# Kernel optimization log

Measured on AMD Instinct MI355X. Metric: run time of the kernel, lower is better.

Reference implementation:

```python
import jax, jax.numpy as jnp
import numpy as np

N_NODES = 50000
N_EDGES = 600000
N_GRAPHS = 512
HID = 128
N_CLASSES = 10
N_LAYERS = 4
BN_EPS = 1e-5


def setup_inputs() -> dict:
    key = jax.random.key(0)
    ks = jax.random.split(key, 12)
    s = 1.0 / np.sqrt(HID)
    x = jax.random.normal(ks[0], (N_NODES, HID), dtype=jnp.float32)
    edge_index = jax.random.randint(ks[1], (2, N_EDGES), 0, N_NODES, dtype=jnp.int64)
    batch = jnp.sort(jax.random.randint(ks[2], (N_NODES,), 0, N_GRAPHS, dtype=jnp.int64))
    return {
        "x": x,
        "edge_index": edge_index,
        "batch": batch,
        # stacked SAGEConv params: lin_l (neighbor, with bias) and lin_r (root, no bias)
        "Wl": jax.random.uniform(ks[3], (N_LAYERS, HID, HID), jnp.float32, -s, s),
        "bl": jax.random.uniform(ks[4], (N_LAYERS, HID), jnp.float32, -s, s),
        "Wr": jax.random.uniform(ks[5], (N_LAYERS, HID, HID), jnp.float32, -s, s),
        # BatchNorm affine params per layer
        "gamma": jnp.ones((N_LAYERS, HID), jnp.float32),
        "beta": jnp.zeros((N_LAYERS, HID), jnp.float32),
        # classifier: Linear(HID, HID//2) -> ReLU -> Linear(HID//2, C)
        "W1": jax.random.uniform(ks[6], (HID // 2, HID), jnp.float32, -s, s),
        "b1": jax.random.uniform(ks[7], (HID // 2,), jnp.float32, -s, s),
        "W2": jax.random.uniform(ks[8], (N_CLASSES, HID // 2), jnp.float32, -1.0 / np.sqrt(HID // 2), 1.0 / np.sqrt(HID // 2)),
        "b2": jax.random.uniform(ks[9], (N_CLASSES,), jnp.float32, -1.0 / np.sqrt(HID // 2), 1.0 / np.sqrt(HID // 2)),
    }


def reference(x, edge_index, batch, Wl, bl, Wr, gamma, beta, W1, b1, W2, b2):
    src, dst = edge_index[0], edge_index[1]
    n = x.shape[0]
    # in-degree for mean aggregation (clamped to avoid div by zero)
    deg = jax.ops.segment_sum(jnp.ones(src.shape[0], x.dtype), dst, num_segments=n)
    inv_deg = 1.0 / jnp.maximum(deg, 1.0)  # [N]
    for l in range(Wl.shape[0]):
        # SAGEConv: mean-aggregate neighbor features, then lin_l(agg) + lin_r(x)
        agg = jax.ops.segment_sum(x[src], dst, num_segments=n) * inv_deg[:, None]  # [N,H]
        h = agg @ Wl[l].T + bl[l] + x @ Wr[l].T  # [N,H]
        # BatchNorm1d (training-mode batch stats, biased variance)
        mu = h.mean(axis=0)
        var = h.var(axis=0)
        h = (h - mu) * jax.lax.rsqrt(var + BN_EPS) * gamma[l] + beta[l]
        x = jax.nn.relu(h)  # dropout is identity in eval/reference
    # global mean pool over graphs
    cnt = jax.ops.segment_sum(jnp.ones(n, x.dtype), batch, num_segments=N_GRAPHS)
    pooled = jax.ops.segment_sum(x, batch, num_segments=N_GRAPHS) / jnp.maximum(cnt, 1.0)[:, None]
    h = jax.nn.relu(pooled @ W1.T + b1)
    return h @ W2.T + b2  # [G, C]
```

## Files before the change

### kernel.cpp

```cpp
#include <hip/hip_runtime.h>

#define NNODES 50000
#define MPAD   50048
#define NEDGES 600000
#define NGRAPHS 512
#define HID 128
#define NLAYERS 4
#define BN_EPS 1e-5f
#define GEMMBLK 391
#define PROWS 25

typedef __bf16 bf16x8 __attribute__((ext_vector_type(8)));
typedef float  f32x4  __attribute__((ext_vector_type(4)));
typedef unsigned short u16x8 __attribute__((ext_vector_type(8)));

__device__ __forceinline__ unsigned short f2bf(float f) {
    unsigned u = __builtin_bit_cast(unsigned, f);
    unsigned r = (u + 0x7fffu + ((u >> 16) & 1u)) >> 16;
    return (unsigned short)r;
}
__device__ __forceinline__ float bf2f(unsigned short u) {
    return __builtin_bit_cast(float, (unsigned)u << 16);
}

__global__ void k_count_deg(const int* __restrict__ dst, int* __restrict__ deg, int E) {
    int e = blockIdx.x * blockDim.x + threadIdx.x;
    if (e < E) atomicAdd(&deg[dst[e]], 1);
}

__global__ void k_scan1(const int* __restrict__ deg, int* __restrict__ exg,
                        int* __restrict__ bsum, int n) {
    __shared__ int s[512];
    int tid = threadIdx.x;
    int i = blockIdx.x * 512 + tid;
    int v = (i < n) ? deg[i] : 0;
    s[tid] = v;
    __syncthreads();
    for (int off = 1; off < 512; off <<= 1) {
        int t = (tid >= off) ? s[tid - off] : 0;
        __syncthreads();
        s[tid] += t;
        __syncthreads();
    }
    if (i < n) exg[i] = s[tid] - v;
    if (tid == 511) bsum[blockIdx.x] = s[511];
}

__global__ void k_scan2(int* __restrict__ bsum, int nb) {
    __shared__ int s[128];
    int tid = threadIdx.x;
    int v = (tid < nb) ? bsum[tid] : 0;
    s[tid] = v;
    __syncthreads();
    for (int off = 1; off < 128; off <<= 1) {
        int t = (tid >= off) ? s[tid - off] : 0;
        __syncthreads();
        s[tid] += t;
        __syncthreads();
    }
    if (tid < nb) bsum[tid] = s[tid] - v;
}

__global__ void k_scan3(const int* __restrict__ exg, const int* __restrict__ bsum,
                        const int* __restrict__ deg,
                        int* __restrict__ rowptr, int* __restrict__ cursor,
                        float* __restrict__ inv_deg, int n, int E) {
    int i = blockIdx.x * blockDim.x + threadIdx.x;
    if (i < n) {
        int r = exg[i] + bsum[i >> 9];
        rowptr[i] = r;
        cursor[i] = r;
        int d = deg[i];
        inv_deg[i] = 1.0f / (float)max(d, 1);
        if (i == 0) rowptr[n] = E;
    }
}

__global__ void k_fill_csr(const int* __restrict__ src, const int* __restrict__ dst,
                           int* __restrict__ cursor, int* __restrict__ csr_src, int E) {
    int e = blockIdx.x * blockDim.x + threadIdx.x;
    if (e < E) {
        int pos = atomicAdd(&cursor[dst[e]], 1);
        csr_src[pos] = src[e];
    }
}

__global__ void k_split(const float* __restrict__ x,
                        unsigned short* __restrict__ xhi, unsigned short* __restrict__ xlo) {
    int idx = blockIdx.x * 256 + threadIdx.x;
    float4 v = ((const float4*)x)[idx];
    ushort4 h, l;
    h.x = f2bf(v.x); l.x = f2bf(v.x - bf2f(h.x));
    h.y = f2bf(v.y); l.y = f2bf(v.y - bf2f(h.y));
    h.z = f2bf(v.z); l.z = f2bf(v.z - bf2f(h.z));
    h.w = f2bf(v.w); l.w = f2bf(v.w - bf2f(h.w));
    *(ushort4*)(xhi + (size_t)idx * 4) = h;
    *(ushort4*)(xlo + (size_t)idx * 4) = l;
}

__global__ void k_wpack(const float* __restrict__ Wl, const float* __restrict__ Wr,
                        unsigned short* __restrict__ Wpk) {
    int lane = threadIdx.x;
    int b = blockIdx.x;
    int nf = b & 7, ks = (b >> 3) & 7, l = b >> 6;
    int n = nf * 16 + (lane & 15);
    int k = ks * 32 + (lane >> 4) * 8;
    const float* W = (k < 128) ? (Wl + (size_t)l * HID * HID)
                               : (Wr + (size_t)l * HID * HID - 128);
    size_t base = ((((size_t)l * 64 + ks * 8 + nf) * 2) * 64 + lane) * 8;
    #pragma unroll
    for (int j = 0; j < 8; ++j) {
        float w = W[(size_t)n * 128 + k + j];
        unsigned short h = f2bf(w);
        unsigned short lo = f2bf(w - bf2f(h));
        Wpk[base + j] = h;
        Wpk[base + 512 + j] = lo;
    }
}

__global__ void k_aggregate4(const unsigned short* __restrict__ xhi,
                             const int* __restrict__ csr_src, const int* __restrict__ rowptr,
                             const float* __restrict__ inv_deg,
                             unsigned short* __restrict__ ahi, unsigned short* __restrict__ alo) {
    int lane = threadIdx.x & 63;
    int wid = threadIdx.x >> 6;
    int node = blockIdx.x * 4 + wid;
    int beg = rowptr[node];
    int end = rowptr[node + 1];
    int eg = lane >> 4;
    int fo = (lane & 15) * 8;
    float acc[8] = {0.f, 0.f, 0.f, 0.f, 0.f, 0.f, 0.f, 0.f};
    int e = beg;
    for (; e + 4 <= end; e += 4) {
        int s = csr_src[e + eg];
        u16x8 v = *(const u16x8*)(xhi + (size_t)s * 128 + fo);
        #pragma unroll
        for (int j = 0; j < 8; ++j) acc[j] += bf2f(v[j]);
    }
    int rem = end - e;
    if (eg < rem) {
        int s = csr_src[e + eg];
        u16x8 v = *(const u16x8*)(xhi + (size_t)s * 128 + fo);
        #pragma unroll
        for (int j = 0; j < 8; ++j) acc[j] += bf2f(v[j]);
    }
    #pragma unroll
    for (int j = 0; j < 8; ++j) {
        acc[j] += __shfl_xor(acc[j], 16);
        acc[j] += __shfl_xor(acc[j], 32);
    }
    if (lane < 16) {
        float idg = inv_deg[node];
        u16x8 hv, lv;
        #pragma unroll
        for (int j = 0; j < 8; ++j) {
            float a = acc[j] * idg;
            unsigned short h = f2bf(a);
            hv[j] = h;
            lv[j] = f2bf(a - bf2f(h));
        }
        *(u16x8*)(ahi + (size_t)node * 128 + fo) = hv;
        *(u16x8*)(alo + (size_t)node * 128 + fo) = lv;
    }
}

__launch_bounds__(256) __global__
void k_mfma_gemm(const unsigned short* __restrict__ Ahi0, const unsigned short* __restrict__ Alo0,
                 const unsigned short* __restrict__ Ahi1, const unsigned short* __restrict__ Alo1,
                 const unsigned short* __restrict__ Wpk, const float* __restrict__ bl,
                 float* __restrict__ Hout,
                 float* __restrict__ psum, float* __restrict__ pqsum) {
    int wid = threadIdx.x >> 6;
    int lane = threadIdx.x & 63;
    int m0 = blockIdx.x * 128 + wid * 32;
    int r = lane & 15;
    int kg = lane >> 4;

    f32x4 acc[2][8];
    #pragma unroll
    for (int nf = 0; nf < 8; ++nf) {
        float b = bl[nf * 16 + r];
        acc[0][nf] = f32x4{b, b, b, b};
        acc[1][nf] = f32x4{b, b, b, b};
    }

    #pragma unroll
    for (int ks = 0; ks < 8; ++ks) {
        const unsigned short* hi = (ks < 4) ? Ahi0 : Ahi1;
        const unsigned short* lo = (ks < 4) ? Alo0 : Alo1;
        int kc = (ks & 3) * 32 + kg * 8;
        bf16x8 ah0 = *(const bf16x8*)(hi + (size_t)(m0 + r) * 128 + kc);
        bf16x8 al0 = *(const bf16x8*)(lo + (size_t)(m0 + r) * 128 + kc);
        bf16x8 ah1 = *(const bf16x8*)(hi + (size_t)(m0 + 16 + r) * 128 + kc);
        bf16x8 al1 = *(const bf16x8*)(lo + (size_t)(m0 + 16 + r) * 128 + kc);
        const unsigned short* wb = Wpk + (size_t)ks * 8192;
        #pragma unroll
        for (int nf = 0; nf < 8; ++nf) {
            bf16x8 bh = *(const bf16x8*)(wb + (size_t)nf * 1024 + lane * 8);
            bf16x8 bl2 = *(const bf16x8*)(wb + (size_t)nf * 1024 + 512 + lane * 8);
            acc[0][nf] = __builtin_amdgcn_mfma_f32_16x16x32_bf16(ah0, bh,  acc[0][nf], 0, 0, 0);
            acc[0][nf] = __builtin_amdgcn_mfma_f32_16x16x32_bf16(al0, bh,  acc[0][nf], 0, 0, 0);
            acc[0][nf] = __builtin_amdgcn_mfma_f32_16x16x32_bf16(ah0, bl2, acc[0][nf], 0, 0, 0);
            acc[1][nf] = __builtin_amdgcn_mfma_f32_16x16x32_bf16(ah1, bh,  acc[1][nf], 0, 0, 0);
            acc[1][nf] = __builtin_amdgcn_mfma_f32_16x16x32_bf16(al1, bh,  acc[1][nf], 0, 0, 0);
            acc[1][nf] = __builtin_amdgcn_mfma_f32_16x16x32_bf16(ah1, bl2, acc[1][nf], 0, 0, 0);
        }
    }

    #pragma unroll
    for (int mf = 0; mf < 2; ++mf)
        #pragma unroll
        for (int nf = 0; nf < 8; ++nf)
            #pragma unroll
            for (int g = 0; g < 4; ++g)
                Hout[(size_t)(m0 + mf * 16 + kg * 4 + g) * 128 + nf * 16 + r] = acc[mf][nf][g];

    __shared__ float ls[4][8][16];
    __shared__ float lq[4][8][16];
    #pragma unroll
    for (int nf = 0; nf < 8; ++nf) {
        float ss = 0.f, qq = 0.f;
        #pragma unroll
        for (int mf = 0; mf < 2; ++mf)
            #pragma unroll
            for (int g = 0; g < 4; ++g) {
                int row = m0 + mf * 16 + kg * 4 + g;
                float v = acc[mf][nf][g];
                float msk = (row < NNODES) ? 1.f : 0.f;
                ss += v * msk;
                qq += v * v * msk;
            }
        ss += __shfl_xor(ss, 16);
        ss += __shfl_xor(ss, 32);
        qq += __shfl_xor(qq, 16);
        qq += __shfl_xor(qq, 32);
        if (lane < 16) { ls[wid][nf][lane] = ss; lq[wid][nf][lane] = qq; }
    }
    __syncthreads();
    int t = threadIdx.x;
    if (t < 128) {
        int nf = t >> 4, rr = t & 15;
        float ssum = ls[0][nf][rr] + ls[1][nf][rr] + ls[2][nf][rr] + ls[3][nf][rr];
        float qsum = lq[0][nf][rr] + lq[1][nf][rr] + lq[2][nf][rr] + lq[3][nf][rr];
        psum[(size_t)t * GEMMBLK + blockIdx.x] = ssum;
        pqsum[(size_t)t * GEMMBLK + blockIdx.x] = qsum;
    }
}

__global__ void k_bnfin2(const float* __restrict__ psum, const float* __restrict__ pqsum,
                         const float* __restrict__ gamma, const float* __restrict__ beta,
                         float* __restrict__ scale, float* __restrict__ shift) {
    int c = blockIdx.x;
    int t = threadIdx.x;
    float s = 0.f, q = 0.f;
    const float* ps = psum + (size_t)c * GEMMBLK;
    const float* pq = pqsum + (size_t)c * GEMMBLK;
    for (int b = t; b < GEMMBLK; b += 64) { s += ps[b]; q += pq[b]; }
    #pragma unroll
    for (int off = 32; off; off >>= 1) {
        s += __shfl_xor(s, off);
        q += __shfl_xor(q, off);
    }
    if (t == 0) {
        float inv_n = 1.0f / (float)NNODES;
        float mu = s * inv_n;
        float var = q * inv_n - mu * mu;
        float is = rsqrtf(var + BN_EPS);
        float g = gamma[c] * is;
        scale[c] = g;
        shift[c] = beta[c] - mu * g;
    }
}

__global__ void k_bnrelu2(const float* __restrict__ h, const float* __restrict__ scale,
                          const float* __restrict__ shift,
                          unsigned short* __restrict__ xhi, unsigned short* __restrict__ xlo) {
    int idx = blockIdx.x * 256 + threadIdx.x;
    int cv = idx & 31;
    float4 sc = ((const float4*)scale)[cv];
    float4 sh = ((const float4*)shift)[cv];
    float4 v = ((const float4*)h)[idx];
    v.x = fmaxf(v.x * sc.x + sh.x, 0.f);
    v.y = fmaxf(v.y * sc.y + sh.y, 0.f);
    v.z = fmaxf(v.z * sc.z + sh.z, 0.f);
    v.w = fmaxf(v.w * sc.w + sh.w, 0.f);
    ushort4 hh, ll;
    hh.x = f2bf(v.x); ll.x = f2bf(v.x - bf2f(hh.x));
    hh.y = f2bf(v.y); ll.y = f2bf(v.y - bf2f(hh.y));
    hh.z = f2bf(v.z); ll.z = f2bf(v.z - bf2f(hh.z));
    hh.w = f2bf(v.w); ll.w = f2bf(v.w - bf2f(hh.w));
    *(ushort4*)(xhi + (size_t)idx * 4) = hh;
    *(ushort4*)(xlo + (size_t)idx * 4) = ll;
}

__global__ void k_pool_seg(const unsigned short* __restrict__ xhi,
                           const unsigned short* __restrict__ xlo,
                           const int* __restrict__ batch,
                           float* __restrict__ pooled, int* __restrict__ gcnt) {
    int t = threadIdx.x;
    int r0 = blockIdx.x * PROWS;
    float a0 = 0.f, a1 = 0.f;
    int cur = batch[r0];
    int seg = r0;
    for (int i = 0; i < PROWS; ++i) {
        int r = r0 + i;
        int g = batch[r];
        if (g != cur) {
            atomicAdd(&pooled[cur * 128 + 2 * t], a0);
            atomicAdd(&pooled[cur * 128 + 2 * t + 1], a1);
            if (t == 0) atomicAdd(&gcnt[cur], r - seg);
            a0 = a1 = 0.f; cur = g; seg = r;
        }
        unsigned uh = *(const unsigned*)(xhi + (size_t)r * 128 + 2 * t);
        unsigned ul = *(const unsigned*)(xlo + (size_t)r * 128 + 2 * t);
        a0 += bf2f((unsigned short)(uh & 0xffff)) + bf2f((unsigned short)(ul & 0xffff));
        a1 += bf2f((unsigned short)(uh >> 16)) + bf2f((unsigned short)(ul >> 16));
    }
    atomicAdd(&pooled[cur * 128 + 2 * t], a0);
    atomicAdd(&pooled[cur * 128 + 2 * t + 1], a1);
    if (t == 0) atomicAdd(&gcnt[cur], r0 + PROWS - seg);
}

__global__ void k_cls(const float* __restrict__ pooled, const int* __restrict__ gcnt,
                      const float* __restrict__ W1, const float* __restrict__ b1,
                      const float* __restrict__ W2, const float* __restrict__ b2,
                      float* __restrict__ out) {
    int g = blockIdx.x;
    int t = threadIdx.x;
    __shared__ float P[128];
    __shared__ float H1[64];
    float inv = 1.0f / (float)max(gcnt[g], 1);
    P[t] = pooled[g * 128 + t] * inv;
    P[t + 64] = pooled[g * 128 + 64 + t] * inv;
    __syncthreads();
    float a = b1[t];
    #pragma unroll 8
    for (int k = 0; k < 128; ++k) a += P[k] * W1[t * 128 + k];
    H1[t] = fmaxf(a, 0.f);
    __syncthreads();
    if (t < 10) {
        float a2 = b2[t];
        #pragma unroll 8
        for (int k = 0; k < 64; ++k) a2 += H1[k] * W2[t * 64 + k];
        out[g * 10 + t] = a2;
    }
}

extern "C" void kernel_launch(void* const* d_in, const int* in_sizes, int n_in,
                              void* d_out, int out_size, void* d_ws, size_t ws_size,
                              hipStream_t stream) {
    const float* x_in  = (const float*)d_in[0];
    const int*   ei    = (const int*)d_in[1];
    const int*   batch = (const int*)d_in[2];
    const float* Wl    = (const float*)d_in[3];
    const float* bl    = (const float*)d_in[4];
    const float* Wr    = (const float*)d_in[5];
    const float* gamma = (const float*)d_in[6];
    const float* beta  = (const float*)d_in[7];
    const float* W1    = (const float*)d_in[8];
    const float* b1    = (const float*)d_in[9];
    const float* W2    = (const float*)d_in[10];
    const float* b2    = (const float*)d_in[11];
    float* out = (float*)d_out;

    const int N = NNODES, E = NEDGES;
    const int* src = ei;
    const int* dst = ei + E;

    char* p = (char*)d_ws;
    auto alloc = [&](size_t bytes) {
        char* r = p;
        p += (bytes + 255) & ~(size_t)255;
        return r;
    };
    unsigned short* ahi = (unsigned short*)alloc((size_t)MPAD * HID * 2);
    unsigned short* alo = (unsigned short*)alloc((size_t)MPAD * HID * 2);
    unsigned short* xhi = (unsigned short*)alloc((size_t)MPAD * HID * 2);
    unsigned short* xlo = (unsigned short*)alloc((size_t)MPAD * HID * 2);
    float*  h        = (float*)alloc((size_t)MPAD * HID * 4);
    unsigned short* wpk = (unsigned short*)alloc((size_t)NLAYERS * 64 * 2 * 64 * 8 * 2);
    int*    deg      = (int*)alloc((size_t)N * 4);
    float*  inv_deg  = (float*)alloc((size_t)N * 4);
    int*    rowptr   = (int*)alloc((size_t)(N + 1) * 4);
    int*    cursor   = (int*)alloc((size_t)N * 4);
    int*    csr_src  = (int*)alloc((size_t)E * 4);
    int*    exg      = (int*)alloc((size_t)N * 4);
    int*    bsum     = (int*)alloc(512);
    float*  psum     = (float*)alloc((size_t)HID * GEMMBLK * 4);
    float*  pqsum    = (float*)alloc((size_t)HID * GEMMBLK * 4);
    float*  scale    = (float*)alloc(HID * 4);
    float*  shift    = (float*)alloc(HID * 4);
    float*  pooled   = (float*)alloc((size_t)NGRAPHS * HID * 4);
    int*    gcnt     = (int*)alloc((size_t)NGRAPHS * 4);

    size_t padbytes = (size_t)(MPAD - N) * HID * 2;
    hipMemsetAsync(ahi + N * HID, 0, padbytes, stream);
    hipMemsetAsync(alo + N * HID, 0, padbytes, stream);
    hipMemsetAsync(xhi + N * HID, 0, padbytes, stream);
    hipMemsetAsync(xlo + N * HID, 0, padbytes, stream);

    hipMemsetAsync(deg, 0, (size_t)N * 4, stream);
    int eb = (E + 255) / 256;
    k_count_deg<<<eb, 256, 0, stream>>>(dst, deg, E);
    int nb = (N + 511) / 512;
    k_scan1<<<nb, 512, 0, stream>>>(deg, exg, bsum, N);
    k_scan2<<<1, 128, 0, stream>>>(bsum, nb);
    k_scan3<<<(N + 255) / 256, 256, 0, stream>>>(exg, bsum, deg, rowptr, cursor, inv_deg, N, E);
    k_fill_csr<<<eb, 256, 0, stream>>>(src, dst, cursor, csr_src, E);

    k_wpack<<<NLAYERS * 64, 64, 0, stream>>>(Wl, Wr, wpk);
    k_split<<<(N * HID / 4) / 256, 256, 0, stream>>>(x_in, xhi, xlo);

    for (int l = 0; l < NLAYERS; ++l) {
        k_aggregate4<<<N / 4, 256, 0, stream>>>(xhi, csr_src, rowptr, inv_deg, ahi, alo);
        k_mfma_gemm<<<GEMMBLK, 256, 0, stream>>>(ahi, alo, xhi, xlo,
                                                 wpk + (size_t)l * 65536,
                                                 bl + (size_t)l * HID, h, psum, pqsum);
        k_bnfin2<<<HID, 64, 0, stream>>>(psum, pqsum, gamma + (size_t)l * HID,
                                         beta + (size_t)l * HID, scale, shift);
        k_bnrelu2<<<(N * HID / 4) / 256, 256, 0, stream>>>(h, scale, shift, xhi, xlo);
    }

    hipMemsetAsync(pooled, 0, (size_t)NGRAPHS * HID * 4, stream);
    hipMemsetAsync(gcnt, 0, (size_t)NGRAPHS * 4, stream);
    k_pool_seg<<<N / PROWS, 64, 0, stream>>>(xhi, xlo, batch, pooled, gcnt);
    k_cls<<<NGRAPHS, 64, 0, stream>>>(pooled, gcnt, W1, b1, W2, b2, out);
}
```

Measured before the change: 402.9 us.

## Preload neighbor indices via shuffles in aggregation and fuse memsets into one init kernel

The aggregation kernel now has each lane load one CSR neighbor index up front and broadcasts it with shuffles. It processes 8 neighbors per iteration into two accumulator sets, which raises memory-level parallelism and removes dependent index loads before the gather. Nodes with more than 64 neighbors fall back to direct index loads. Seven hipMemsetAsync calls are replaced by one init kernel that zeroes the degree array, the padding rows, the pooled buffer and the graph counts, cutting launch overhead. This adds more registers and branch divergence per lane.

```diff
diff --git a/kernel.cpp b/kernel.cpp
--- a/kernel.cpp
+++ b/kernel.cpp
@@ -21,6 +21,20 @@
 }
 __device__ __forceinline__ float bf2f(unsigned short u) {
     return __builtin_bit_cast(float, (unsigned)u << 16);
+}
+
+__global__ void k_init(int* __restrict__ deg,
+                       int* __restrict__ pa, int* __restrict__ pb,
+                       int* __restrict__ pc, int* __restrict__ pd,
+                       int* __restrict__ pooled, int* __restrict__ gcnt) {
+    int t = blockIdx.x * 256 + threadIdx.x;
+    if (t < 50000) { deg[t] = 0; }
+    int u = t - 50000;
+    if (u >= 0 && u < 3072) { pa[u] = 0; pb[u] = 0; pc[u] = 0; pd[u] = 0; }
+    int v = t - 53072;
+    if (v >= 0 && v < 65536) pooled[v] = 0;
+    int w = t - 118608;
+    if (w >= 0 && w < 512) gcnt[w] = 0;
 }
 
 __global__ void k_count_deg(const int* __restrict__ dst, int* __restrict__ deg, int E) {
@@ -118,7 +132,7 @@
     }
 }
 
-__global__ void k_aggregate4(const unsigned short* __restrict__ xhi,
+__global__ void k_aggregate5(const unsigned short* __restrict__ xhi,
                              const int* __restrict__ csr_src, const int* __restrict__ rowptr,
                              const float* __restrict__ inv_deg,
                              unsigned short* __restrict__ ahi, unsigned short* __restrict__ alo) {
@@ -126,35 +140,49 @@
     int wid = threadIdx.x >> 6;
     int node = blockIdx.x * 4 + wid;
     int beg = rowptr[node];
-    int end = rowptr[node + 1];
+    int deg = rowptr[node + 1] - beg;
     int eg = lane >> 4;
     int fo = (lane & 15) * 8;
-    float acc[8] = {0.f, 0.f, 0.f, 0.f, 0.f, 0.f, 0.f, 0.f};
-    int e = beg;
-    for (; e + 4 <= end; e += 4) {
-        int s = csr_src[e + eg];
+
+    int idx_l = (lane < deg) ? csr_src[beg + lane] : 0;
+
+    float acc0[8] = {0.f, 0.f, 0.f, 0.f, 0.f, 0.f, 0.f, 0.f};
+    float acc1[8] = {0.f, 0.f, 0.f, 0.f, 0.f, 0.f, 0.f, 0.f};
+    int dmax = min(deg, 64);
+    for (int base = 0; base < dmax; base += 8) {
+        int s0 = __shfl(idx_l, base + eg);
+        int s1 = __shfl(idx_l, base + 4 + eg);
+        if (base + eg < deg) {
+            u16x8 v = *(const u16x8*)(xhi + (size_t)s0 * 128 + fo);
+            #pragma unroll
+            for (int j = 0; j < 8; ++j) acc0[j] += bf2f(v[j]);
+        }
+        if (base + 4 + eg < deg) {
+            u16x8 v = *(const u16x8*)(xhi + (size_t)s1 * 128 + fo);
+            #pragma unroll
+            for (int j = 0; j < 8; ++j) acc1[j] += bf2f(v[j]);
+        }
+    }
+    for (int e = beg + 64 + eg; e < beg + deg; e += 4) {
+        int s = csr_src[e];
         u16x8 v = *(const u16x8*)(xhi + (size_t)s * 128 + fo);
         #pragma unroll
-        for (int j = 0; j < 8; ++j) acc[j] += bf2f(v[j]);
-    }
-    int rem = end - e;
-    if (eg < rem) {
-        int s = csr_src[e + eg];
-        u16x8 v = *(const u16x8*)(xhi + (size_t)s * 128 + fo);
-        #pragma unroll
-        for (int j = 0; j < 8; ++j) acc[j] += bf2f(v[j]);
-    }
+        for (int j = 0; j < 8; ++j) acc0[j] += bf2f(v[j]);
+    }
+
     #pragma unroll
     for (int j = 0; j < 8; ++j) {
-        acc[j] += __shfl_xor(acc[j], 16);
-        acc[j] += __shfl_xor(acc[j], 32);
+        float a = acc0[j] + acc1[j];
+        a += __shfl_xor(a, 16);
+        a += __shfl_xor(a, 32);
+        acc0[j] = a;
     }
     if (lane < 16) {
         float idg = inv_deg[node];
         u16x8 hv, lv;
         #pragma unroll
         for (int j = 0; j < 8; ++j) {
-            float a = acc[j] * idg;
+            float a = acc0[j] * idg;
             unsigned short h = f2bf(a);
             hv[j] = h;
             lv[j] = f2bf(a - bf2f(h));
@@ -393,13 +421,11 @@
     float*  pooled   = (float*)alloc((size_t)NGRAPHS * HID * 4);
     int*    gcnt     = (int*)alloc((size_t)NGRAPHS * 4);
 
-    size_t padbytes = (size_t)(MPAD - N) * HID * 2;
-    hipMemsetAsync(ahi + N * HID, 0, padbytes, stream);
-    hipMemsetAsync(alo + N * HID, 0, padbytes, stream);
-    hipMemsetAsync(xhi + N * HID, 0, padbytes, stream);
-    hipMemsetAsync(xlo + N * HID, 0, padbytes, stream);
-
-    hipMemsetAsync(deg, 0, (size_t)N * 4, stream);
+    k_init<<<502, 256, 0, stream>>>(deg,
+                                    (int*)(ahi + (size_t)N * HID), (int*)(alo + (size_t)N * HID),
+                                    (int*)(xhi + (size_t)N * HID), (int*)(xlo + (size_t)N * HID),
+                                    (int*)pooled, gcnt);
+
     int eb = (E + 255) / 256;
     k_count_deg<<<eb, 256, 0, stream>>>(dst, deg, E);
     int nb = (N + 511) / 512;
@@ -412,7 +438,7 @@
     k_split<<<(N * HID / 4) / 256, 256, 0, stream>>>(x_in, xhi, xlo);
 
     for (int l = 0; l < NLAYERS; ++l) {
-        k_aggregate4<<<N / 4, 256, 0, stream>>>(xhi, csr_src, rowptr, inv_deg, ahi, alo);
+        k_aggregate5<<<N / 4, 256, 0, stream>>>(xhi, csr_src, rowptr, inv_deg, ahi, alo);
         k_mfma_gemm<<<GEMMBLK, 256, 0, stream>>>(ahi, alo, xhi, xlo,
                                                  wpk + (size_t)l * 65536,
                                                  bl + (size_t)l * HID, h, psum, pqsum);
@@ -421,8 +447,6 @@
         k_bnrelu2<<<(N * HID / 4) / 256, 256, 0, stream>>>(h, scale, shift, xhi, xlo);
     }
 
-    hipMemsetAsync(pooled, 0, (size_t)NGRAPHS * HID * 4, stream);
-    hipMemsetAsync(gcnt, 0, (size_t)NGRAPHS * 4, stream);
     k_pool_seg<<<N / PROWS, 64, 0, stream>>>(xhi, xlo, batch, pooled, gcnt);
     k_cls<<<NGRAPHS, 64, 0, stream>>>(pooled, gcnt, W1, b1, W2, b2, out);
 }
```

New measurement: 379.4 us. 1.06x faster.
